# Kernel optimization log

Hardware: AMD Instinct MI355X
Metric: run time of the kernel (lower is better)

## Reference

```python
import jax, jax.numpy as jnp
import numpy as np

N_NODES = 100_000
N_EDGES = 20_000   # hyperedges
NNZ = 2_000_000    # incidence pairs
F = 128
BN_EPS = 1e-5


def setup_inputs() -> dict:
    key = jax.random.key(0)
    ks = jax.random.split(key, 6)
    x_0 = jax.random.normal(ks[0], (N_NODES, F), dtype=jnp.float32)
    x_1 = jax.random.normal(ks[1], (N_EDGES, F), dtype=jnp.float32)
    node_idx = jax.random.randint(ks[2], (NNZ,), 0, N_NODES, dtype=jnp.int32)
    edge_idx = jax.random.randint(ks[3], (NNZ,), 0, N_EDGES, dtype=jnp.int32)
    W_nh = jax.random.normal(ks[4], (F, F), dtype=jnp.float32) / np.float32(np.sqrt(F))
    b_nh = jnp.zeros((F,), jnp.float32)
    W_en = jax.random.normal(ks[5], (F, 2 * F), dtype=jnp.float32) / np.float32(np.sqrt(2 * F))
    b_en = jnp.zeros((F,), jnp.float32)
    ones = jnp.ones((F,), jnp.float32)
    zeros = jnp.zeros((F,), jnp.float32)
    return {
        "x_0": x_0, "x_1": x_1, "node_idx": node_idx, "edge_idx": edge_idx,
        "W_nh": W_nh, "b_nh": b_nh, "W_en": W_en, "b_en": b_en,
        "bn0_gamma": ones, "bn0_beta": zeros, "bn0_mean": zeros, "bn0_var": ones,
        "bn1_gamma": ones, "bn1_beta": zeros, "bn1_mean": zeros, "bn1_var": ones,
    }


def _bn_eval(x, gamma, beta, mean, var):
    # BatchNorm1d in eval mode: normalize with running stats.
    return (x - mean) * (gamma * jax.lax.rsqrt(var + BN_EPS)) + beta


def reference(x_0, x_1, node_idx, edge_idx, W_nh, b_nh, W_en, b_en,
              bn0_gamma, bn0_beta, bn0_mean, bn0_var,
              bn1_gamma, bn1_beta, bn1_mean, bn1_var):
    # --- node -> hyperedge messenger ---
    # per-node message: sigmoid(Linear(x_0))  [n_nodes, F]
    node_messages = jax.nn.sigmoid(x_0 @ W_nh.T + b_nh)
    # gather over incidence list, scatter-sum onto hyperedges  [n_edges, F]
    node_msg_agg = jax.ops.segment_sum(node_messages[node_idx], edge_idx,
                                       num_segments=N_EDGES)

    # --- hyperedge -> node messenger ---
    # per-hyperedge message: sigmoid(Linear(cat(x_1, agg node msgs)))  [n_edges, F]
    he_messages = jax.nn.sigmoid(
        jnp.concatenate([x_1, node_msg_agg], axis=1) @ W_en.T + b_en)
    # gather per incidence, scatter-sum onto nodes  [n_nodes, F]
    he_msg_agg = jax.ops.segment_sum(he_messages[edge_idx], node_idx,
                                     num_segments=N_NODES)

    # --- updates (eval mode: feature dropout is identity) ---
    x0_out = jax.nn.sigmoid(
        _bn_eval(x_0, bn0_gamma, bn0_beta, bn0_mean, bn0_var) + he_msg_agg)
    x1_out = jax.nn.sigmoid(
        _bn_eval(x_1, bn1_gamma, bn1_beta, bn1_mean, bn1_var) + node_msg_agg)
    return (x0_out, x1_out)
```

## Files before the change

kernel.cpp:

```cpp
#include <hip/hip_runtime.h>
#include <hip/hip_bf16.h>
#include <math.h>

#define NNODES 100000
#define NEDGES 20000
#define NNZ_   2000000
#define FDIM   128
#define BN_EPS 1e-5f

#define NBUCK 256
#define CAP   9216
#define BPB_E 79
#define BPB_N 391
#define SH_E  17
#define SH_N  15
#define NPART 8
#define PSLICE 12500

typedef __attribute__((ext_vector_type(8))) short bf16x8_t;
typedef __attribute__((ext_vector_type(4))) float f32x4_t;
typedef __attribute__((ext_vector_type(8))) unsigned short u16x8_t;

__device__ __forceinline__ float sigmoidf_(float x) {
    return 1.0f / (1.0f + __expf(-x));
}
__device__ __forceinline__ float bf2f(unsigned short u) {
    return __uint_as_float(((unsigned)u) << 16);
}
__device__ __forceinline__ unsigned short f2bf(float f) {
    __hip_bfloat16 h = __float2bfloat16(f);
    return *reinterpret_cast<unsigned short*>(&h);
}

__global__ __launch_bounds__(256) void prep_w(
    const float* __restrict__ W_nh, const float* __restrict__ W_en,
    unsigned short* __restrict__ Wnh_bf, float* __restrict__ WTen)
{
    int idx = blockIdx.x * blockDim.x + threadIdx.x;
    if (idx < FDIM * FDIM) {
        Wnh_bf[idx] = f2bf(W_nh[idx]);
    } else {
        int j = idx - FDIM * FDIM;
        if (j >= 2 * FDIM * FDIM) return;
        int k = j >> 7, c = j & 127;
        WTen[j] = W_en[c * 2 * FDIM + k];
    }
}

__global__ __launch_bounds__(256) void gemm1_mfma(
    const float* __restrict__ x0, const unsigned short* __restrict__ Wb,
    const float* __restrict__ bias, unsigned short* __restrict__ out)
{
    __shared__ unsigned short As[32][FDIM + 8];
    const int tid  = threadIdx.x;
    const int row0 = blockIdx.x * 32;
    {
        int r = tid >> 3, c0 = (tid & 7) * 16;
        const float* src = x0 + (size_t)(row0 + r) * FDIM + c0;
        unsigned short* dst = &As[r][c0];
        #pragma unroll
        for (int i = 0; i < 4; i++) {
            float4 v = *(const float4*)(src + i * 4);
            dst[i * 4 + 0] = f2bf(v.x);
            dst[i * 4 + 1] = f2bf(v.y);
            dst[i * 4 + 2] = f2bf(v.z);
            dst[i * 4 + 3] = f2bf(v.w);
        }
    }
    __syncthreads();
    const int wave  = tid >> 6;
    const int lane  = tid & 63;
    const int mhalf = wave & 1;
    const int nhalf = wave >> 1;
    const int lm    = lane & 15;
    const int quad  = lane >> 4;
    f32x4_t acc[4] = {};
    #pragma unroll
    for (int ks = 0; ks < 4; ks++) {
        bf16x8_t a = *(const bf16x8_t*)&As[mhalf * 16 + lm][ks * 32 + quad * 8];
        #pragma unroll
        for (int nt = 0; nt < 4; nt++) {
            int n = nhalf * 64 + nt * 16 + lm;
            bf16x8_t b = *(const bf16x8_t*)(Wb + (size_t)n * FDIM + ks * 32 + quad * 8);
            acc[nt] = __builtin_amdgcn_mfma_f32_16x16x32_bf16(a, b, acc[nt], 0, 0, 0);
        }
    }
    const int mbase = row0 + mhalf * 16 + quad * 4;
    #pragma unroll
    for (int nt = 0; nt < 4; nt++) {
        int n = nhalf * 64 + nt * 16 + lm;
        float bv = bias[n];
        #pragma unroll
        for (int r2 = 0; r2 < 4; r2++) {
            out[(size_t)(mbase + r2) * FDIM + n] = f2bf(sigmoidf_(acc[nt][r2] + bv));
        }
    }
}

__global__ __launch_bounds__(256, 2) void gemm_sig_bf16(
    const float* __restrict__ A1, const float* __restrict__ A2,
    const float* __restrict__ WT, const float* __restrict__ bias,
    unsigned short* __restrict__ out)
{
    constexpr int K = 256, BK = 64;
    __shared__ float As[32][BK + 4];
    __shared__ float Ws[BK][FDIM];
    const int tid  = threadIdx.x;
    const int row0 = blockIdx.x * 32;
    const int tcol = tid & 31;
    const int trow = tid >> 5;
    float acc[4][4] = {};
    for (int kk = 0; kk < K; kk += BK) {
        const float* Asrc = (kk < FDIM) ? A1 : A2;
        const int koff    = (kk < FDIM) ? kk : kk - FDIM;
        #pragma unroll
        for (int i = 0; i < 2; i++) {
            int l = tid + i * 256;
            int r = l >> 4, j = l & 15;
            float4 v = *(const float4*)(Asrc + (size_t)(row0 + r) * FDIM + koff + j * 4);
            *(float4*)&As[r][j * 4] = v;
        }
        #pragma unroll
        for (int i = 0; i < 8; i++) {
            int l = tid + i * 256;
            int k = l >> 5, j = l & 31;
            float4 v = *(const float4*)(WT + (size_t)(kk + k) * FDIM + j * 4);
            *(float4*)&Ws[k][j * 4] = v;
        }
        __syncthreads();
        #pragma unroll
        for (int k = 0; k < BK; k += 4) {
            float4 a[4];
            #pragma unroll
            for (int r = 0; r < 4; r++)
                a[r] = *(const float4*)&As[trow * 4 + r][k];
            #pragma unroll
            for (int kq = 0; kq < 4; kq++) {
                float4 w = *(const float4*)&Ws[k + kq][tcol * 4];
                #pragma unroll
                for (int r = 0; r < 4; r++) {
                    float av = (kq == 0) ? a[r].x : (kq == 1) ? a[r].y
                             : (kq == 2) ? a[r].z : a[r].w;
                    acc[r][0] += av * w.x;
                    acc[r][1] += av * w.y;
                    acc[r][2] += av * w.z;
                    acc[r][3] += av * w.w;
                }
            }
        }
        __syncthreads();
    }
    float4 bv = *(const float4*)(bias + tcol * 4);
    #pragma unroll
    for (int r = 0; r < 4; r++) {
        int row = row0 + trow * 4 + r;
        ushort4 o;
        o.x = f2bf(sigmoidf_(acc[r][0] + bv.x));
        o.y = f2bf(sigmoidf_(acc[r][1] + bv.y));
        o.z = f2bf(sigmoidf_(acc[r][2] + bv.z));
        o.w = f2bf(sigmoidf_(acc[r][3] + bv.w));
        *(ushort4*)(out + (size_t)row * FDIM + tcol * 4) = o;
    }
}

__global__ __launch_bounds__(256, 2) void gemm2_fused(
    const float* __restrict__ A1, const float* __restrict__ part,
    const float* __restrict__ WT, const float* __restrict__ bias,
    const float* __restrict__ g1, const float* __restrict__ b1,
    const float* __restrict__ m1, const float* __restrict__ v1,
    float* __restrict__ out1, unsigned short* __restrict__ outD)
{
    constexpr int K = 256, BK = 64;
    __shared__ float As[32][BK + 4];
    __shared__ float Ws[BK][FDIM];
    const int tid  = threadIdx.x;
    const int row0 = blockIdx.x * 32;
    const int tcol = tid & 31;
    const int trow = tid >> 5;
    float acc[4][4] = {};
    for (int kk = 0; kk < K; kk += BK) {
        if (kk < FDIM) {
            #pragma unroll
            for (int i = 0; i < 2; i++) {
                int l = tid + i * 256;
                int r = l >> 4, j = l & 15;
                float4 v = *(const float4*)(A1 + (size_t)(row0 + r) * FDIM + kk + j * 4);
                *(float4*)&As[r][j * 4] = v;
            }
        } else {
            const int koff = kk - FDIM;
            #pragma unroll
            for (int i = 0; i < 2; i++) {
                int l = tid + i * 256;
                int r = l >> 4, j = l & 15;
                int col = koff + j * 4;
                const float* pp = part + (size_t)(row0 + r) * FDIM + col;
                f32x4_t bsum = {};
                #pragma unroll
                for (int p = 0; p < NPART; p++)
                    bsum += *(const f32x4_t*)(pp + (size_t)p * NEDGES * FDIM);
                *(f32x4_t*)&As[r][j * 4] = bsum;
                f32x4_t xv = *(const f32x4_t*)(A1 + (size_t)(row0 + r) * FDIM + col);
                f32x4_t gg = *(const f32x4_t*)(g1 + col);
                f32x4_t bt = *(const f32x4_t*)(b1 + col);
                f32x4_t mn = *(const f32x4_t*)(m1 + col);
                f32x4_t vr = *(const f32x4_t*)(v1 + col);
                f32x4_t o;
                #pragma unroll
                for (int jj = 0; jj < 4; jj++)
                    o[jj] = sigmoidf_((xv[jj] - mn[jj]) * (gg[jj] * rsqrtf(vr[jj] + BN_EPS))
                                      + bt[jj] + bsum[jj]);
                *(f32x4_t*)(out1 + (size_t)(row0 + r) * FDIM + col) = o;
            }
        }
        #pragma unroll
        for (int i = 0; i < 8; i++) {
            int l = tid + i * 256;
            int k = l >> 5, j = l & 31;
            float4 v = *(const float4*)(WT + (size_t)(kk + k) * FDIM + j * 4);
            *(float4*)&Ws[k][j * 4] = v;
        }
        __syncthreads();
        #pragma unroll
        for (int k = 0; k < BK; k += 4) {
            float4 a[4];
            #pragma unroll
            for (int r = 0; r < 4; r++)
                a[r] = *(const float4*)&As[trow * 4 + r][k];
            #pragma unroll
            for (int kq = 0; kq < 4; kq++) {
                float4 w = *(const float4*)&Ws[k + kq][tcol * 4];
                #pragma unroll
                for (int r = 0; r < 4; r++) {
                    float av = (kq == 0) ? a[r].x : (kq == 1) ? a[r].y
                             : (kq == 2) ? a[r].z : a[r].w;
                    acc[r][0] += av * w.x;
                    acc[r][1] += av * w.y;
                    acc[r][2] += av * w.z;
                    acc[r][3] += av * w.w;
                }
            }
        }
        __syncthreads();
    }
    float4 bv = *(const float4*)(bias + tcol * 4);
    #pragma unroll
    for (int r = 0; r < 4; r++) {
        int row = row0 + trow * 4 + r;
        ushort4 o;
        o.x = f2bf(sigmoidf_(acc[r][0] + bv.x));
        o.y = f2bf(sigmoidf_(acc[r][1] + bv.y));
        o.z = f2bf(sigmoidf_(acc[r][2] + bv.z));
        o.w = f2bf(sigmoidf_(acc[r][3] + bv.w));
        *(ushort4*)(outD + (size_t)row * FDIM + tcol * 4) = o;
    }
}

__global__ __launch_bounds__(1024) void bucket_scatter(
    const int* __restrict__ ni, const int* __restrict__ ei,
    unsigned* __restrict__ buck_e, unsigned* __restrict__ buck_n,
    int* __restrict__ gcur_e, int* __restrict__ gcur_n)
{
    __shared__ int lh_e[NBUCK], lh_n[NBUCK], lb_e[NBUCK], lb_n[NBUCK];
    const int t = threadIdx.x;
    if (t < NBUCK) { lh_e[t] = 0; lh_n[t] = 0; }
    __syncthreads();
    unsigned ent_e[4], ent_n[4];
    int be[4], bn[4], re[4], rn[4];
    const int base = blockIdx.x * 4096;
    #pragma unroll
    for (int j = 0; j < 4; j++) {
        int i = base + j * 1024 + t;
        if (i < NNZ_) {
            unsigned n = (unsigned)ni[i], e = (unsigned)ei[i];
            ent_e[j] = (e << SH_E) | n;  be[j] = (int)(e / BPB_E);
            ent_n[j] = (n << SH_N) | e;  bn[j] = (int)(n / BPB_N);
            re[j] = atomicAdd(&lh_e[be[j]], 1);
            rn[j] = atomicAdd(&lh_n[bn[j]], 1);
        } else { be[j] = -1; }
    }
    __syncthreads();
    if (t < NBUCK) {
        lb_e[t] = t * CAP + atomicAdd(&gcur_e[t], lh_e[t]);
        lb_n[t] = t * CAP + atomicAdd(&gcur_n[t], lh_n[t]);
    }
    __syncthreads();
    #pragma unroll
    for (int j = 0; j < 4; j++) {
        if (be[j] >= 0) {
            buck_e[(size_t)lb_e[be[j]] + re[j]] = ent_e[j];
            buck_n[(size_t)lb_n[bn[j]] + rn[j]] = ent_n[j];
        }
    }
}

__device__ __forceinline__ int ep_bin(unsigned ent) {
    int e = (int)(ent >> SH_E);
    int n = (int)(ent & 0x1FFFFu);
    return e * NPART + n / PSLICE;
}

__device__ __forceinline__ void sort_bucket_e(
    const unsigned* __restrict__ region, int cnt, int gbase, int bucket,
    unsigned* __restrict__ csr, int* __restrict__ off)
{
    __shared__ unsigned lh[768];
    __shared__ unsigned lw[4];
    const int t = threadIdx.x;
    lh[t] = 0; lh[t + 256] = 0; lh[t + 512] = 0;
    __syncthreads();
    const int b0 = bucket * (BPB_E * NPART);
    for (int i = t; i < cnt; i += 256)
        atomicAdd(&lh[ep_bin(region[i]) - b0], 1u);
    __syncthreads();
    unsigned h0 = lh[3 * t], h1 = lh[3 * t + 1], h2 = lh[3 * t + 2];
    unsigned s = h0 + h1 + h2, inc = s;
    const int lane = t & 63;
    #pragma unroll
    for (int d = 1; d <= 32; d <<= 1) {
        unsigned v = (unsigned)__shfl_up((int)inc, d, 64);
        if (lane >= d) inc += v;
    }
    if (lane == 63) lw[t >> 6] = inc;
    __syncthreads();
    unsigned pre = 0;
    #pragma unroll
    for (int w = 0; w < 4; w++) if (w < (t >> 6)) pre += lw[w];
    unsigned excl = pre + inc - s;
    unsigned c0 = (unsigned)gbase + excl, c1 = c0 + h0, c2 = c1 + h1;
    lh[3 * t] = c0; lh[3 * t + 1] = c1; lh[3 * t + 2] = c2;
    #pragma unroll
    for (int j = 0; j < 3; j++) {
        int ib = 3 * t + j;
        unsigned cc = (j == 0) ? c0 : (j == 1) ? c1 : c2;
        if (ib <= BPB_E * NPART && b0 + ib <= NEDGES * NPART) off[b0 + ib] = (int)cc;
    }
    __syncthreads();
    for (int i = t; i < cnt; i += 256) {
        unsigned ent = region[i];
        unsigned pos = atomicAdd(&lh[ep_bin(ent) - b0], 1u);
        csr[pos] = ent & 0x1FFFFu;
    }
}

__device__ __forceinline__ void sort_bucket_n(
    const unsigned* __restrict__ region, int cnt, int gbase, int b0,
    unsigned short* __restrict__ csr, int* __restrict__ off)
{
    __shared__ unsigned lh[512];
    __shared__ unsigned lw[4];
    const int t = threadIdx.x;
    lh[t] = 0; lh[t + 256] = 0;
    __syncthreads();
    for (int i = t; i < cnt; i += 256) {
        int bin = (int)(region[i] >> SH_N) - b0;
        atomicAdd(&lh[bin], 1u);
    }
    __syncthreads();
    unsigned h0 = lh[2 * t], h1 = lh[2 * t + 1];
    unsigned s = h0 + h1, inc = s;
    const int lane = t & 63;
    #pragma unroll
    for (int d = 1; d <= 32; d <<= 1) {
        unsigned v = (unsigned)__shfl_up((int)inc, d, 64);
        if (lane >= d) inc += v;
    }
    if (lane == 63) lw[t >> 6] = inc;
    __syncthreads();
    unsigned pre = 0;
    #pragma unroll
    for (int w = 0; w < 4; w++) if (w < (t >> 6)) pre += lw[w];
    unsigned excl = pre + inc - s;
    unsigned c0 = (unsigned)gbase + excl;
    unsigned c1 = c0 + h0;
    lh[2 * t] = c0; lh[2 * t + 1] = c1;
    int i0 = 2 * t, i1 = 2 * t + 1;
    if (i0 <= BPB_N && b0 + i0 <= NNODES) off[b0 + i0] = (int)c0;
    if (i1 <= BPB_N && b0 + i1 <= NNODES) off[b0 + i1] = (int)c1;
    __syncthreads();
    for (int i = t; i < cnt; i += 256) {
        unsigned ent = region[i];
        int bin = (int)(ent >> SH_N) - b0;
        unsigned pos = atomicAdd(&lh[bin], 1u);
        csr[pos] = (unsigned short)(ent & 0x7FFFu);
    }
}

__global__ __launch_bounds__(256) void bucket_sort(
    const unsigned* __restrict__ buck_e, const unsigned* __restrict__ buck_n,
    const int* __restrict__ gcur_e, const int* __restrict__ gcur_n,
    unsigned* __restrict__ csr_e, unsigned short* __restrict__ csr_n,
    int* __restrict__ off_ep, int* __restrict__ off_n)
{
    const int b = blockIdx.x & 255;
    const int* gc = (blockIdx.x < 256) ? gcur_e : gcur_n;
    __shared__ int ws4[4];
    const int t = threadIdx.x;
    int v = (t < b) ? gc[t] : 0;
    #pragma unroll
    for (int d = 32; d > 0; d >>= 1) v += __shfl_down(v, d, 64);
    if ((t & 63) == 0) ws4[t >> 6] = v;
    __syncthreads();
    const int gbase = ws4[0] + ws4[1] + ws4[2] + ws4[3];
    const int cnt = gc[b];
    __syncthreads();
    if (blockIdx.x < 256)
        sort_bucket_e(buck_e + (size_t)b * CAP, cnt, gbase, b, csr_e, off_ep);
    else
        sort_bucket_n(buck_n + (size_t)b * CAP, cnt, gbase, b * BPB_N, csr_n, off_n);
}

__global__ __launch_bounds__(256) void seg_part_gather(
    const unsigned short* __restrict__ table, const unsigned* __restrict__ csr,
    const int* __restrict__ off_ep, float* __restrict__ partial)
{
    const int p = blockIdx.x & 7;
    const int e = (blockIdx.x >> 3) * 4 + (threadIdx.x >> 6);
    const int lane = threadIdx.x & 63;
    const int sub  = lane >> 4;
    const int c8   = (lane & 15) * 8;
    const int bin  = e * NPART + p;
    const int i0 = off_ep[bin], i1 = off_ep[bin + 1];
    f32x4_t a0 = {}, a1 = {};
    for (int i = i0; i < i1; i += 16) {
        u16x8_t v[4];
        #pragma unroll
        for (int u = 0; u < 4; u++) {
            int row_i = i + 4 * u + sub;
            u16x8_t z = {};
            v[u] = z;
            if (row_i < i1)
                v[u] = *(const u16x8_t*)(table + (size_t)csr[row_i] * FDIM + c8);
        }
        #pragma unroll
        for (int u = 0; u < 4; u++) {
            a0[0] += bf2f(v[u][0]); a0[1] += bf2f(v[u][1]);
            a0[2] += bf2f(v[u][2]); a0[3] += bf2f(v[u][3]);
            a1[0] += bf2f(v[u][4]); a1[1] += bf2f(v[u][5]);
            a1[2] += bf2f(v[u][6]); a1[3] += bf2f(v[u][7]);
        }
    }
    #pragma unroll
    for (int j = 0; j < 4; j++) {
        a0[j] += __shfl_xor(a0[j], 16, 64);
        a0[j] += __shfl_xor(a0[j], 32, 64);
        a1[j] += __shfl_xor(a1[j], 16, 64);
        a1[j] += __shfl_xor(a1[j], 32, 64);
    }
    if (sub < 2) {
        const int q = c8 + sub * 4;
        f32x4_t s = sub ? a1 : a0;
        *(f32x4_t*)(partial + ((size_t)p * NEDGES + e) * FDIM + q) = s;
    }
}

template<typename IDX, int U, int OFFSTR>
__global__ __launch_bounds__(256) void seg_sum_fin_v2(
    const unsigned short* __restrict__ table, const IDX* __restrict__ csr,
    const int* __restrict__ off, const float* __restrict__ x,
    const float* __restrict__ g, const float* __restrict__ bb,
    const float* __restrict__ mm, const float* __restrict__ vv,
    float* __restrict__ agg_out, float* __restrict__ fin_out, int nseg)
{
    const int seg = blockIdx.x * 4 + (threadIdx.x >> 6);
    if (seg >= nseg) return;
    const int lane = threadIdx.x & 63;
    const int c    = lane & 15;
    const int sub  = lane >> 4;
    const int c8   = c * 8;

    const int i0 = off[seg * OFFSTR], i1 = off[seg * OFFSTR + OFFSTR];
    f32x4_t a0 = {}, a1 = {};

    int i = i0;
    for (; i + 4 * U <= i1; i += 4 * U) {
        int r[U];
        u16x8_t v[U];
        #pragma unroll
        for (int u = 0; u < U; u++) r[u] = (int)csr[i + 4 * u + sub];
        #pragma unroll
        for (int u = 0; u < U; u++)
            v[u] = *(const u16x8_t*)(table + (size_t)r[u] * FDIM + c8);
        #pragma unroll
        for (int u = 0; u < U; u++) {
            a0[0] += bf2f(v[u][0]); a0[1] += bf2f(v[u][1]);
            a0[2] += bf2f(v[u][2]); a0[3] += bf2f(v[u][3]);
            a1[0] += bf2f(v[u][4]); a1[1] += bf2f(v[u][5]);
            a1[2] += bf2f(v[u][6]); a1[3] += bf2f(v[u][7]);
        }
    }
    if (i < i1) {
        u16x8_t v[U];
        #pragma unroll
        for (int u = 0; u < U; u++) {
            int row = i + 4 * u + sub;
            u16x8_t z = {};
            v[u] = z;
            if (row < i1)
                v[u] = *(const u16x8_t*)(table + (size_t)csr[row] * FDIM + c8);
        }
        #pragma unroll
        for (int u = 0; u < U; u++) {
            a0[0] += bf2f(v[u][0]); a0[1] += bf2f(v[u][1]);
            a0[2] += bf2f(v[u][2]); a0[3] += bf2f(v[u][3]);
            a1[0] += bf2f(v[u][4]); a1[1] += bf2f(v[u][5]);
            a1[2] += bf2f(v[u][6]); a1[3] += bf2f(v[u][7]);
        }
    }

    #pragma unroll
    for (int j = 0; j < 4; j++) {
        a0[j] += __shfl_xor(a0[j], 16, 64);
        a0[j] += __shfl_xor(a0[j], 32, 64);
        a1[j] += __shfl_xor(a1[j], 16, 64);
        a1[j] += __shfl_xor(a1[j], 32, 64);
    }

    if (sub < 2) {
        const int q = c8 + sub * 4;
        f32x4_t s = sub ? a1 : a0;
        if (agg_out)
            *(f32x4_t*)(agg_out + (size_t)seg * FDIM + q) = s;
        if (fin_out) {
            f32x4_t xv = *(const f32x4_t*)(x + (size_t)seg * FDIM + q);
            f32x4_t gg = *(const f32x4_t*)(g + q);
            f32x4_t bt = *(const f32x4_t*)(bb + q);
            f32x4_t mn = *(const f32x4_t*)(mm + q);
            f32x4_t vr = *(const f32x4_t*)(vv + q);
            f32x4_t o;
            #pragma unroll
            for (int j = 0; j < 4; j++)
                o[j] = sigmoidf_((xv[j] - mn[j]) * (gg[j] * rsqrtf(vr[j] + BN_EPS))
                                 + bt[j] + s[j]);
            *(f32x4_t*)(fin_out + (size_t)seg * FDIM + q) = o;
        }
    }
}

extern "C" void kernel_launch(void* const* d_in, const int* in_sizes, int n_in,
                              void* d_out, int out_size, void* d_ws, size_t ws_size,
                              hipStream_t stream)
{
    const float* x0       = (const float*)d_in[0];
    const float* x1       = (const float*)d_in[1];
    const int*   node_idx = (const int*)d_in[2];
    const int*   edge_idx = (const int*)d_in[3];
    const float* W_nh     = (const float*)d_in[4];
    const float* b_nh     = (const float*)d_in[5];
    const float* W_en     = (const float*)d_in[6];
    const float* b_en     = (const float*)d_in[7];
    const float* bn0g = (const float*)d_in[8];
    const float* bn0b = (const float*)d_in[9];
    const float* bn0m = (const float*)d_in[10];
    const float* bn0v = (const float*)d_in[11];
    const float* bn1g = (const float*)d_in[12];
    const float* bn1b = (const float*)d_in[13];
    const float* bn1m = (const float*)d_in[14];
    const float* bn1v = (const float*)d_in[15];

    float* ws = (float*)d_ws;
    float* B    = ws;
    float* WTen = B + (size_t)NEDGES * FDIM;
    unsigned short* Wnh_bf = (unsigned short*)(WTen + 2 * FDIM * FDIM);
    unsigned short* A_bf = Wnh_bf + FDIM * FDIM;
    unsigned short* D_bf = A_bf + (size_t)NNODES * FDIM;
    int* off_ep = (int*)(D_bf + (size_t)NEDGES * FDIM);
    int* off_n  = off_ep + 160004;
    unsigned* csr_e = (unsigned*)(off_n + 100004);
    unsigned short* csr_n = (unsigned short*)(csr_e + NNZ_);
    unsigned* buck_e = (unsigned*)(csr_n + NNZ_);
    unsigned* buck_n = buck_e + (size_t)NBUCK * CAP;
    int* gcur_e = (int*)(buck_n + (size_t)NBUCK * CAP);
    int* gcur_n = gcur_e + NBUCK;
    float* partial = (float*)buck_e;
    const size_t need = ((char*)partial - (char*)d_ws)
                      + (size_t)NPART * NEDGES * FDIM * sizeof(float);
    const bool big = ws_size >= need;

    hipMemsetAsync(gcur_e, 0, 2 * NBUCK * sizeof(int), stream);
    bucket_scatter<<<(NNZ_ + 4095) / 4096, 1024, 0, stream>>>(
        node_idx, edge_idx, buck_e, buck_n, gcur_e, gcur_n);
    bucket_sort<<<2 * NBUCK, 256, 0, stream>>>(buck_e, buck_n, gcur_e, gcur_n,
                                               csr_e, csr_n, off_ep, off_n);

    prep_w<<<(3 * FDIM * FDIM + 255) / 256, 256, 0, stream>>>(W_nh, W_en, Wnh_bf, WTen);

    float* out0 = (float*)d_out;
    float* out1 = out0 + (size_t)NNODES * FDIM;

    gemm1_mfma<<<NNODES / 32, 256, 0, stream>>>(x0, Wnh_bf, b_nh, A_bf);

    if (big) {
        seg_part_gather<<<(NEDGES / 4) * 8, 256, 0, stream>>>(
            A_bf, csr_e, off_ep, partial);
        gemm2_fused<<<NEDGES / 32, 256, 0, stream>>>(
            x1, partial, WTen, b_en, bn1g, bn1b, bn1m, bn1v, out1, D_bf);
    } else {
        seg_sum_fin_v2<unsigned, 8, NPART><<<(NEDGES + 3) / 4, 256, 0, stream>>>(
            A_bf, csr_e, off_ep, x1, bn1g, bn1b, bn1m, bn1v, B, out1, NEDGES);
        gemm_sig_bf16<<<NEDGES / 32, 256, 0, stream>>>(x1, B, WTen, b_en, D_bf);
    }

    seg_sum_fin_v2<unsigned short, 4, 1><<<(NNODES + 3) / 4, 256, 0, stream>>>(
        D_bf, csr_n, off_n, x0, bn0g, bn0b, bn0m, bn0v, nullptr, out0, NNODES);
}
```

Before: 423.3 us.

## Split fused partial-reduce GEMM into reduce kernel plus bf16 GEMM; add nontemporal accesses

Removes the fp32 SIMT gemm2_fused kernel, which reduced the per-partition partials inside the GEMM load stage. A new elementwise reduce_fin kernel now sums the partials, writes B and the x1 output, and the existing gemm_sig_bf16 path runs afterwards. Index loads and streaming outputs in the gather kernels now use nontemporal loads and stores to reduce cache pollution. The split adds one launch and a round trip of B through memory, in exchange for a likely faster GEMM and a bandwidth-friendly reduction.

Result: slower. 437.2 us (+3.3%).

```diff
diff --git a/kernel.cpp b/kernel.cpp
--- a/kernel.cpp
+++ b/kernel.cpp
@@ -163,99 +163,6 @@
     }
 }
 
-__global__ __launch_bounds__(256, 2) void gemm2_fused(
-    const float* __restrict__ A1, const float* __restrict__ part,
-    const float* __restrict__ WT, const float* __restrict__ bias,
-    const float* __restrict__ g1, const float* __restrict__ b1,
-    const float* __restrict__ m1, const float* __restrict__ v1,
-    float* __restrict__ out1, unsigned short* __restrict__ outD)
-{
-    constexpr int K = 256, BK = 64;
-    __shared__ float As[32][BK + 4];
-    __shared__ float Ws[BK][FDIM];
-    const int tid  = threadIdx.x;
-    const int row0 = blockIdx.x * 32;
-    const int tcol = tid & 31;
-    const int trow = tid >> 5;
-    float acc[4][4] = {};
-    for (int kk = 0; kk < K; kk += BK) {
-        if (kk < FDIM) {
-            #pragma unroll
-            for (int i = 0; i < 2; i++) {
-                int l = tid + i * 256;
-                int r = l >> 4, j = l & 15;
-                float4 v = *(const float4*)(A1 + (size_t)(row0 + r) * FDIM + kk + j * 4);
-                *(float4*)&As[r][j * 4] = v;
-            }
-        } else {
-            const int koff = kk - FDIM;
-            #pragma unroll
-            for (int i = 0; i < 2; i++) {
-                int l = tid + i * 256;
-                int r = l >> 4, j = l & 15;
-                int col = koff + j * 4;
-                const float* pp = part + (size_t)(row0 + r) * FDIM + col;
-                f32x4_t bsum = {};
-                #pragma unroll
-                for (int p = 0; p < NPART; p++)
-                    bsum += *(const f32x4_t*)(pp + (size_t)p * NEDGES * FDIM);
-                *(f32x4_t*)&As[r][j * 4] = bsum;
-                f32x4_t xv = *(const f32x4_t*)(A1 + (size_t)(row0 + r) * FDIM + col);
-                f32x4_t gg = *(const f32x4_t*)(g1 + col);
-                f32x4_t bt = *(const f32x4_t*)(b1 + col);
-                f32x4_t mn = *(const f32x4_t*)(m1 + col);
-                f32x4_t vr = *(const f32x4_t*)(v1 + col);
-                f32x4_t o;
-                #pragma unroll
-                for (int jj = 0; jj < 4; jj++)
-                    o[jj] = sigmoidf_((xv[jj] - mn[jj]) * (gg[jj] * rsqrtf(vr[jj] + BN_EPS))
-                                      + bt[jj] + bsum[jj]);
-                *(f32x4_t*)(out1 + (size_t)(row0 + r) * FDIM + col) = o;
-            }
-        }
-        #pragma unroll
-        for (int i = 0; i < 8; i++) {
-            int l = tid + i * 256;
-            int k = l >> 5, j = l & 31;
-            float4 v = *(const float4*)(WT + (size_t)(kk + k) * FDIM + j * 4);
-            *(float4*)&Ws[k][j * 4] = v;
-        }
-        __syncthreads();
-        #pragma unroll
-        for (int k = 0; k < BK; k += 4) {
-            float4 a[4];
-            #pragma unroll
-            for (int r = 0; r < 4; r++)
-                a[r] = *(const float4*)&As[trow * 4 + r][k];
-            #pragma unroll
-            for (int kq = 0; kq < 4; kq++) {
-                float4 w = *(const float4*)&Ws[k + kq][tcol * 4];
-                #pragma unroll
-                for (int r = 0; r < 4; r++) {
-                    float av = (kq == 0) ? a[r].x : (kq == 1) ? a[r].y
-                             : (kq == 2) ? a[r].z : a[r].w;
-                    acc[r][0] += av * w.x;
-                    acc[r][1] += av * w.y;
-                    acc[r][2] += av * w.z;
-                    acc[r][3] += av * w.w;
-                }
-            }
-        }
-        __syncthreads();
-    }
-    float4 bv = *(const float4*)(bias + tcol * 4);
-    #pragma unroll
-    for (int r = 0; r < 4; r++) {
-        int row = row0 + trow * 4 + r;
-        ushort4 o;
-        o.x = f2bf(sigmoidf_(acc[r][0] + bv.x));
-        o.y = f2bf(sigmoidf_(acc[r][1] + bv.y));
-        o.z = f2bf(sigmoidf_(acc[r][2] + bv.z));
-        o.w = f2bf(sigmoidf_(acc[r][3] + bv.w));
-        *(ushort4*)(outD + (size_t)row * FDIM + tcol * 4) = o;
-    }
-}
-
 __global__ __launch_bounds__(1024) void bucket_scatter(
     const int* __restrict__ ni, const int* __restrict__ ei,
     unsigned* __restrict__ buck_e, unsigned* __restrict__ buck_n,
@@ -429,8 +336,10 @@
             int row_i = i + 4 * u + sub;
             u16x8_t z = {};
             v[u] = z;
-            if (row_i < i1)
-                v[u] = *(const u16x8_t*)(table + (size_t)csr[row_i] * FDIM + c8);
+            if (row_i < i1) {
+                int r = (int)__builtin_nontemporal_load(&csr[row_i]);
+                v[u] = *(const u16x8_t*)(table + (size_t)r * FDIM + c8);
+            }
         }
         #pragma unroll
         for (int u = 0; u < 4; u++) {
@@ -450,8 +359,38 @@
     if (sub < 2) {
         const int q = c8 + sub * 4;
         f32x4_t s = sub ? a1 : a0;
-        *(f32x4_t*)(partial + ((size_t)p * NEDGES + e) * FDIM + q) = s;
-    }
+        __builtin_nontemporal_store(s,
+            (f32x4_t*)(partial + ((size_t)p * NEDGES + e) * FDIM + q));
+    }
+}
+
+__global__ __launch_bounds__(256) void reduce_fin(
+    const float* __restrict__ part, const float* __restrict__ x1,
+    const float* __restrict__ g, const float* __restrict__ bb,
+    const float* __restrict__ mm, const float* __restrict__ vv,
+    float* __restrict__ B, float* __restrict__ out1)
+{
+    const int idx = blockIdx.x * 256 + threadIdx.x;
+    if (idx >= NEDGES * (FDIM / 4)) return;
+    const size_t q = (size_t)idx * 4;
+    f32x4_t s = {};
+    #pragma unroll
+    for (int p = 0; p < NPART; p++)
+        s += __builtin_nontemporal_load(
+                 (const f32x4_t*)(part + (size_t)p * NEDGES * FDIM + q));
+    __builtin_nontemporal_store(s, (f32x4_t*)(B + q));
+    const int col = (idx & 31) * 4;
+    f32x4_t xv = __builtin_nontemporal_load((const f32x4_t*)(x1 + q));
+    f32x4_t gg = *(const f32x4_t*)(g + col);
+    f32x4_t bt = *(const f32x4_t*)(bb + col);
+    f32x4_t mn = *(const f32x4_t*)(mm + col);
+    f32x4_t vr = *(const f32x4_t*)(vv + col);
+    f32x4_t o;
+    #pragma unroll
+    for (int j = 0; j < 4; j++)
+        o[j] = sigmoidf_((xv[j] - mn[j]) * (gg[j] * rsqrtf(vr[j] + BN_EPS))
+                         + bt[j] + s[j]);
+    __builtin_nontemporal_store(o, (f32x4_t*)(out1 + q));
 }
 
 template<typename IDX, int U, int OFFSTR>
@@ -477,7 +416,8 @@
         int r[U];
         u16x8_t v[U];
         #pragma unroll
-        for (int u = 0; u < U; u++) r[u] = (int)csr[i + 4 * u + sub];
+        for (int u = 0; u < U; u++)
+            r[u] = (int)__builtin_nontemporal_load(&csr[i + 4 * u + sub]);
         #pragma unroll
         for (int u = 0; u < U; u++)
             v[u] = *(const u16x8_t*)(table + (size_t)r[u] * FDIM + c8);
@@ -520,9 +460,10 @@
         const int q = c8 + sub * 4;
         f32x4_t s = sub ? a1 : a0;
         if (agg_out)
-            *(f32x4_t*)(agg_out + (size_t)seg * FDIM + q) = s;
+            __builtin_nontemporal_store(s, (f32x4_t*)(agg_out + (size_t)seg * FDIM + q));
         if (fin_out) {
-            f32x4_t xv = *(const f32x4_t*)(x + (size_t)seg * FDIM + q);
+            f32x4_t xv = __builtin_nontemporal_load(
+                             (const f32x4_t*)(x + (size_t)seg * FDIM + q));
             f32x4_t gg = *(const f32x4_t*)(g + q);
             f32x4_t bt = *(const f32x4_t*)(bb + q);
             f32x4_t mn = *(const f32x4_t*)(mm + q);
@@ -532,7 +473,7 @@
             for (int j = 0; j < 4; j++)
                 o[j] = sigmoidf_((xv[j] - mn[j]) * (gg[j] * rsqrtf(vr[j] + BN_EPS))
                                  + bt[j] + s[j]);
-            *(f32x4_t*)(fin_out + (size_t)seg * FDIM + q) = o;
+            __builtin_nontemporal_store(o, (f32x4_t*)(fin_out + (size_t)seg * FDIM + q));
         }
     }
 }
@@ -593,13 +534,13 @@
     if (big) {
         seg_part_gather<<<(NEDGES / 4) * 8, 256, 0, stream>>>(
             A_bf, csr_e, off_ep, partial);
-        gemm2_fused<<<NEDGES / 32, 256, 0, stream>>>(
-            x1, partial, WTen, b_en, bn1g, bn1b, bn1m, bn1v, out1, D_bf);
+        reduce_fin<<<(NEDGES * (FDIM / 4) + 255) / 256, 256, 0, stream>>>(
+            partial, x1, bn1g, bn1b, bn1m, bn1v, B, out1);
     } else {
         seg_sum_fin_v2<unsigned, 8, NPART><<<(NEDGES + 3) / 4, 256, 0, stream>>>(
             A_bf, csr_e, off_ep, x1, bn1g, bn1b, bn1m, bn1v, B, out1, NEDGES);
-        gemm_sig_bf16<<<NEDGES / 32, 256, 0, stream>>>(x1, B, WTen, b_en, D_bf);
-    }
+    }
+    gemm_sig_bf16<<<NEDGES / 32, 256, 0, stream>>>(x1, B, WTen, b_en, D_bf);
 
     seg_sum_fin_v2<unsigned short, 4, 1><<<(NNODES + 3) / 4, 256, 0, stream>>>(
         D_bf, csr_n, off_n, x0, bn0g, bn0b, bn0m, bn0v, nullptr, out0, NNODES);
```
